# Kernel tuning notes

Measured on AMD Instinct MI355X. Metric: run time of the kernel, lower is better.

Reference implementation:

```python
import jax, jax.numpy as jnp
import numpy as np

N = 50000      # nodes
E = 800000     # edges (before self-loops)
F_IN = 128     # args.nsegment
H = 4          # args.nhead
C = 32         # args.dhidden
OUT = 64       # output_dim
G = 64         # number of graphs in batch
NEG = 0.2      # args.negslope (and GATv2 internal leaky-relu slope, PyG default 0.2)


def setup_inputs() -> dict:
    key = jax.random.key(0)
    ks = jax.random.split(key, 8)
    def w(k, i, o):
        return jax.random.normal(k, (i, o), jnp.float32) / np.sqrt(i)
    x = jax.random.normal(ks[0], (N, F_IN), jnp.float32)
    edge_index = jax.random.randint(ks[1], (2, E), 0, N, dtype=jnp.int32)
    batch = jnp.sort(jax.random.randint(ks[2], (N,), 0, G, dtype=jnp.int32))
    d = dict(x=x, edge_index=edge_index, batch=batch)
    # layer dims: (in_dim, heads, out_per_head, concat)
    dims = [(F_IN, H, C, True), (H * C, H, C, True), (H * C, 1, OUT, False)]
    for li, (fi, h, c, concat) in enumerate(dims):
        k1, k2, k3 = jax.random.split(ks[3 + li], 3)
        d[f"Wl{li}"] = w(k1, fi, h * c)
        d[f"Wr{li}"] = w(k2, fi, h * c)
        d[f"att{li}"] = jax.random.normal(k3, (h, c), jnp.float32) / np.sqrt(c)
        d[f"b{li}"] = jnp.zeros((h * c if concat else c,), jnp.float32)
    return d


def _gat_layer(x, src, tgt, Wl, Wr, att, b, concat):
    """GATv2Conv: e_ij = att . leaky_relu(Wl x_j + Wr x_i); softmax over edges into i;
    out_i = sum_j alpha_ij * (Wl x_j). src/tgt include self-loops."""
    n = x.shape[0]
    h, c = att.shape
    xl = (x @ Wl).reshape(n, h, c)                 # source transform [N,h,c]
    xr = (x @ Wr).reshape(n, h, c)                 # target transform [N,h,c]
    g = jax.nn.leaky_relu(xl[src] + xr[tgt], NEG)  # [Etot,h,c]
    score = jnp.einsum('ehc,hc->eh', g, att)       # [Etot,h]
    smax = jax.ops.segment_max(score, tgt, num_segments=n)
    ex = jnp.exp(score - smax[tgt])
    den = jax.ops.segment_sum(ex, tgt, num_segments=n)
    alpha = ex / den[tgt]                          # per-target softmax [Etot,h]
    out = jax.ops.segment_sum(xl[src] * alpha[:, :, None], tgt, num_segments=n)
    out = out.reshape(n, h * c) if concat else out.mean(axis=1)
    return out + b


def _forward(x, edge_index, batch, params):
    n = x.shape[0]
    loops = jnp.arange(n, dtype=edge_index.dtype)  # PyG add_self_loops=True
    src = jnp.concatenate([edge_index[0], loops])
    tgt = jnp.concatenate([edge_index[1], loops])
    for Wl, Wr, att, b, concat in params:
        x = _gat_layer(x, src, tgt, Wl, Wr, att, b, concat)
        x = jax.nn.leaky_relu(x, NEG)  # dropout p is identity in eval mode
    ssum = jax.ops.segment_sum(x, batch, num_segments=G)
    cnt = jax.ops.segment_sum(jnp.ones((n,), x.dtype), batch, num_segments=G)
    return ssum / jnp.maximum(cnt, 1.0)[:, None]   # global_mean_pool -> [G, OUT]


def reference(x, edge_index, batch, Wl0, Wr0, att0, b0, Wl1, Wr1, att1, b1, Wl2, Wr2, att2, b2):
    params = [(Wl0, Wr0, att0, b0, True),
              (Wl1, Wr1, att1, b1, True),
              (Wl2, Wr2, att2, b2, False)]
    return _forward(x, edge_index, batch, params)
```

## Files before the change

### kernel.cpp

```cpp
#include <hip/hip_runtime.h>
#include <hip/hip_fp16.h>
#include <math.h>

#define NEGSLOPE 0.2f

typedef _Float16 f16x8 __attribute__((ext_vector_type(8)));
typedef _Float16 f16x2 __attribute__((ext_vector_type(2)));
typedef float f32x4 __attribute__((ext_vector_type(4)));

__device__ __forceinline__ float lrelu(float x) { return x > 0.f ? x : NEGSLOPE * x; }

__device__ __forceinline__ float dot2acc(f16x2 a, f16x2 b, float c) {
#if __has_builtin(__builtin_amdgcn_fdot2)
    return __builtin_amdgcn_fdot2(a, b, c, false);
#else
    return c + (float)a[0] * (float)b[0] + (float)a[1] * (float)b[1];
#endif
}

__global__ __launch_bounds__(256) void k_prep(
        const float* __restrict__ x, _Float16* __restrict__ xh, int n8, int XB,
        const float* W0, const float* W1, const float* W2,
        const float* W3, const float* W4, const float* W5,
        _Float16* D0, _Float16* D1, _Float16* D2,
        _Float16* D3, _Float16* D4, _Float16* D5,
        int* __restrict__ zbase, int nzero) {
    int b = blockIdx.x, t = threadIdx.x;
    if (b < XB) {
        int i = b * 256 + t;
        if (i < n8) {
            float4 a = ((const float4*)x)[2 * i], c = ((const float4*)x)[2 * i + 1];
            union { uint4 u; _Float16 h[8]; } pk;
            pk.h[0] = (_Float16)a.x; pk.h[1] = (_Float16)a.y;
            pk.h[2] = (_Float16)a.z; pk.h[3] = (_Float16)a.w;
            pk.h[4] = (_Float16)c.x; pk.h[5] = (_Float16)c.y;
            pk.h[6] = (_Float16)c.z; pk.h[7] = (_Float16)c.w;
            ((uint4*)xh)[i] = pk.u;
        }
    } else if (b < XB + 320) {
        const float* Ws[6] = {W0, W1, W2, W3, W4, W5};
        _Float16* Ds[6] = {D0, D1, D2, D3, D4, D5};
        int j = (b - XB) * 256 + t;
        int m, jj, kout;
        if (j < 65536) { m = j >> 14; jj = j & 16383; kout = 128; }
        else           { m = 4 + ((j - 65536) >> 13); jj = (j - 65536) & 8191; kout = 64; }
        int col = jj >> 7, k = jj & 127;
        Ds[m][col * 128 + k] = (_Float16)Ws[m][k * kout + col];
    } else {
        int i = (b - XB - 320) * 256 + t;
        if (i < nzero) zbase[i] = 0;
    }
}

__global__ void k_count(const int* __restrict__ tgt, int* __restrict__ deg,
                        int* __restrict__ rank, int e) {
    int i = blockIdx.x * 256 + threadIdx.x;
    if (i < e) rank[i] = atomicAdd(&deg[tgt[i]], 1);
}
__global__ __launch_bounds__(256) void k_scanA(const int* __restrict__ deg, int* __restrict__ rowptr,
                                               int* __restrict__ bsums, int* __restrict__ bhist, int n) {
    __shared__ int s[256];
    __shared__ int lh[64];
    int t = threadIdx.x;
    if (t < 64) lh[t] = 0;
    int base = blockIdx.x * 4096 + t * 16;
    int pre[16];
    int sum = 0;
    __syncthreads();
    for (int i = 0; i < 16; ++i) {
        int idx = base + i;
        int v = 0;
        if (idx < n) {
            v = deg[idx] + 1;
            atomicAdd(&lh[v < 63 ? v : 63], 1);
        }
        pre[i] = sum;
        sum += v;
    }
    s[t] = sum;
    __syncthreads();
    for (int off = 1; off < 256; off <<= 1) {
        int v = (t >= off) ? s[t - off] : 0;
        __syncthreads();
        s[t] += v;
        __syncthreads();
    }
    int tbase = s[t] - sum;
    for (int i = 0; i < 16; ++i) {
        int idx = base + i;
        if (idx < n) rowptr[idx] = tbase + pre[i];
    }
    if (t == 0) bsums[blockIdx.x] = s[255];
    if (t < 64) bhist[blockIdx.x * 64 + t] = lh[t];
}
__global__ void k_binit(const int* __restrict__ bhist, int* __restrict__ boff, int nscan) {
    __shared__ int tots[64];
    __shared__ int base[64];
    int b = threadIdx.x;
    int tot = 0;
    for (int sb = 0; sb < nscan; ++sb) {
        boff[sb * 64 + b] = tot;
        tot += bhist[sb * 64 + b];
    }
    tots[b] = tot;
    __syncthreads();
    if (b == 0) {
        int run = 0;
        for (int k = 0; k < 64; ++k) { base[k] = run; run += tots[k]; }
    }
    __syncthreads();
    for (int sb = 0; sb < nscan; ++sb) boff[sb * 64 + b] += base[b];
}
__global__ __launch_bounds__(256) void k_scanC(int* __restrict__ rowptr, const int* __restrict__ bsums,
                                               int* __restrict__ edst, const int* __restrict__ deg,
                                               const int* __restrict__ boff, int* __restrict__ perm,
                                               int nscan, int n) {
    __shared__ int pref[17];
    __shared__ int cur[64];
    int t = threadIdx.x;
    if (t == 0) {
        int run = 0;
        for (int k = 0; k < nscan; ++k) { pref[k] = run; run += bsums[k]; }
        pref[nscan] = run;
    }
    if (t < 64) cur[t] = boff[blockIdx.x * 64 + t];
    __syncthreads();
    int myoff = pref[blockIdx.x];
    int base = blockIdx.x * 4096 + t * 16;
    for (int i = 0; i < 16; ++i) {
        int idx = base + i;
        if (idx < n) {
            int rp = rowptr[idx] + myoff;
            rowptr[idx] = rp;
            edst[rp] = idx;
            int d = deg[idx] + 1;
            int slot = atomicAdd(&cur[d < 63 ? d : 63], 1);
            perm[slot] = idx;
        }
    }
    if (blockIdx.x == gridDim.x - 1 && t == 0) rowptr[n] = pref[nscan];
}
__global__ void k_scatter(const int* __restrict__ src, const int* __restrict__ tgt,
                          const int* __restrict__ rank, const int* __restrict__ rowptr,
                          int* __restrict__ edst, int e) {
    int i = blockIdx.x * 256 + threadIdx.x;
    if (i < e) {
        int p = rowptr[tgt[i]] + 1 + rank[i];
        __builtin_nontemporal_store(src[i], &edst[p]);
    }
}

template<int KOUT>
__global__ __launch_bounds__(256) void k_gemm_mfma(
        const _Float16* __restrict__ Ah,
        const _Float16* __restrict__ Wt0, const _Float16* __restrict__ Wt1,
        _Float16* __restrict__ out0, _Float16* __restrict__ out1, int n) {
    int wv = threadIdx.x >> 6, lane = threadIdx.x & 63;
    int m = lane & 15, q = lane >> 4;
    int row0 = blockIdx.x * 128 + wv * 32;
    int ra = row0 + m, rb = row0 + 16 + m;
    if (ra >= n) ra = n - 1;
    if (rb >= n) rb = n - 1;
    const _Float16* apa = Ah + (size_t)ra * 128 + q * 8;
    const _Float16* apb = Ah + (size_t)rb * 128 + q * 8;

    const _Float16* Wp = Wt0;
    _Float16* outp = out0;
    if (KOUT == 128 && blockIdx.y) { Wp = Wt1; outp = out1; }

    f32x4 acc0[8] = {}, acc1[8] = {};
#pragma unroll
    for (int kt = 0; kt < 4; ++kt) {
        f16x8 wf[8];
#pragma unroll
        for (int ct = 0; ct < 8; ++ct) {
            const _Float16* W = (KOUT == 128) ? Wp : (ct < 4 ? Wt0 : Wt1);
            int col0 = (KOUT == 128) ? ct * 16 : (ct & 3) * 16;
            wf[ct] = *(const f16x8*)(W + (size_t)(col0 + m) * 128 + 32 * kt + 8 * q);
        }
        f16x8 bf0 = *(const f16x8*)(apa + 32 * kt);
        f16x8 bf1 = *(const f16x8*)(apb + 32 * kt);
#pragma unroll
        for (int ct = 0; ct < 8; ++ct) {
            acc0[ct] = __builtin_amdgcn_mfma_f32_16x16x32_f16(wf[ct], bf0, acc0[ct], 0, 0, 0);
            acc1[ct] = __builtin_amdgcn_mfma_f32_16x16x32_f16(wf[ct], bf1, acc1[ct], 0, 0, 0);
        }
    }
    int rowa = row0 + m, rowb = row0 + 16 + m;
#pragma unroll
    for (int ct = 0; ct < 8; ++ct) {
        _Float16* dst = (KOUT == 128) ? outp : (ct < 4 ? out0 : out1);
        int col = ((KOUT == 128) ? ct * 16 : (ct & 3) * 16) + q * 4;
        union { uint2 u; _Float16 h[4]; } pk;
        if (rowa < n) {
#pragma unroll
            for (int i = 0; i < 4; ++i) pk.h[i] = (_Float16)acc0[ct][i];
            *(uint2*)(dst + (size_t)rowa * KOUT + col) = pk.u;
        }
        if (rowb < n) {
#pragma unroll
            for (int i = 0; i < 4; ++i) pk.h[i] = (_Float16)acc1[ct][i];
            *(uint2*)(dst + (size_t)rowb * KOUT + col) = pk.u;
        }
    }
}

template<int H, int C, typename OutT>
__global__ __launch_bounds__(256) void k_agg(const _Float16* __restrict__ xl, const _Float16* __restrict__ xr,
                                             const float* __restrict__ att, const float* __restrict__ bias,
                                             const int* __restrict__ rowptr, const int* __restrict__ edst,
                                             const int* __restrict__ perm,
                                             OutT* __restrict__ yout, int n) {
    constexpr int F = H * C;
    constexpr int VEC = F / 16;
    constexpr int NH2 = VEC / 2;
    constexpr int L = C / VEC;
    int lane = threadIdx.x & 63;
    int wave = threadIdx.x >> 6;
    int s = lane & 15;
    int gid = blockIdx.x * 16 + wave * 4 + (lane >> 4);
    bool valid = gid < n;
    int node = valid ? perm[gid] : 0;
    int ch = s * VEC;

    f16x2 u2[NH2], av2[NH2];
    {
        union { uint4 u4; uint2 u2v; f16x2 h[4]; } pk;
        if constexpr (NH2 == 4) pk.u4 = *(const uint4*)(xr + (size_t)node * F + ch);
        else pk.u2v = *(const uint2*)(xr + (size_t)node * F + ch);
#pragma unroll
        for (int j = 0; j < NH2; ++j) u2[j] = pk.h[j];
    }
#pragma unroll
    for (int j = 0; j < NH2; ++j) {
        av2[j][0] = (_Float16)att[ch + 2 * j];
        av2[j][1] = (_Float16)att[ch + 2 * j + 1];
    }

    float acc[VEC];
#pragma unroll
    for (int j = 0; j < VEC; ++j) acc[j] = 0.f;
    int e0 = rowptr[node];
    int deg = valid ? (rowptr[node + 1] - e0) : 0;
    int maxdeg = deg;
    maxdeg = max(maxdeg, __shfl_xor(maxdeg, 16));
    maxdeg = max(maxdeg, __shfl_xor(maxdeg, 32));
    float ssum = 0.f;

    const _Float16 cneg = (_Float16)NEGSLOPE;
    auto edge = [&](int srcRow, bool live) {
        union { uint4 u4; uint2 u2v; f16x2 hh[4]; } pk;
        const _Float16* p = xl + (size_t)srcRow * F + ch;
        if constexpr (NH2 == 4) pk.u4 = *(const uint4*)p;
        else pk.u2v = *(const uint2*)p;
        float sc = 0.f;
#pragma unroll
        for (int j = 0; j < NH2; ++j) {
            f16x2 t = pk.hh[j] + u2[j];
            f16x2 lr = __builtin_elementwise_max(t, t * cneg);
            sc = dot2acc(lr, av2[j], sc);
        }
#pragma unroll
        for (int off = 1; off < L; off <<= 1) sc += __shfl_xor(sc, off);
        float w = live ? __expf(sc) : 0.f;
        ssum += w;
#pragma unroll
        for (int j = 0; j < NH2; ++j) {
            acc[2 * j]     += w * (float)pk.hh[j][0];
            acc[2 * j + 1] += w * (float)pk.hh[j][1];
        }
    };

    for (int base = 0; base < maxdeg; base += 16) {
        int cnt = deg - base;
        if (cnt > 16) cnt = 16;
        int idxreg = (s < cnt) ? edst[e0 + base + s] : node;
        int mcnt = cnt;
        mcnt = max(mcnt, __shfl_xor(mcnt, 16));
        mcnt = max(mcnt, __shfl_xor(mcnt, 32));
        int gbase = lane & 48;
        int i = 0;
        for (; i + 2 <= mcnt; i += 2) {
            int s0 = __shfl(idxreg, gbase + i);
            int s1 = __shfl(idxreg, gbase + i + 1);
            edge(s0, i < cnt);
            edge(s1, i + 1 < cnt);
        }
        for (; i < mcnt; ++i) {
            int s0 = __shfl(idxreg, gbase + i);
            edge(s0, i < cnt);
        }
    }
    if (valid) {
        float inv = 1.f / ssum;
        float o[VEC];
#pragma unroll
        for (int j = 0; j < VEC; ++j) o[j] = lrelu(acc[j] * inv + bias[ch + j]);
        if constexpr (sizeof(OutT) == 2) {
            _Float16* p = (_Float16*)yout + (size_t)node * F + ch;
            if constexpr (VEC == 8) {
                union { uint4 u; _Float16 h[8]; } pk;
#pragma unroll
                for (int j = 0; j < 8; ++j) pk.h[j] = (_Float16)o[j];
                *(uint4*)p = pk.u;
            } else {
                union { uint2 u; _Float16 h[4]; } pk;
#pragma unroll
                for (int j = 0; j < 4; ++j) pk.h[j] = (_Float16)o[j];
                *(uint2*)p = pk.u;
            }
        } else {
            float* p = (float*)yout + (size_t)node * F + ch;
            *(float4*)p = make_float4(o[0], o[1], o[2], o[3]);
            if constexpr (VEC == 8)
                *(float4*)(p + 4) = make_float4(o[4], o[5], o[6], o[7]);
        }
    }
}

__global__ __launch_bounds__(256) void k_pool_partial(const float* __restrict__ y,
        const int* __restrict__ batch, float* __restrict__ pacc, int n, int nchunk) {
    __shared__ float sdata[256];
    __shared__ int range[2];
    int g = blockIdx.x;
    int chunk = blockIdx.y;
    int t = threadIdx.x;
    if (t == 0) {
        int lo = 0, hi = n;
        while (lo < hi) { int mid = (lo + hi) >> 1; if (batch[mid] < g) lo = mid + 1; else hi = mid; }
        range[0] = lo;
        hi = n;
        while (lo < hi) { int mid = (lo + hi) >> 1; if (batch[mid] < g + 1) lo = mid + 1; else hi = mid; }
        range[1] = lo;
    }
    __syncthreads();
    int start = range[0], len = range[1] - range[0];
    int lo = start + (int)((long long)len * chunk / nchunk);
    int hi = start + (int)((long long)len * (chunk + 1) / nchunk);
    int ch = t & 63, sub = t >> 6;
    float acc = 0.f;
    for (int node = lo + sub; node < hi; node += 4)
        acc += y[(size_t)node * 64 + ch];
    sdata[t] = acc;
    __syncthreads();
    if (t < 128) sdata[t] += sdata[t + 128];
    __syncthreads();
    if (t < 64) atomicAdd(&pacc[g * 64 + t], sdata[t] + sdata[t + 64]);
}
__global__ void k_pool_final(const float* __restrict__ pacc, const int* __restrict__ batch,
                             float* __restrict__ out, int n) {
    __shared__ int cntS;
    int g = blockIdx.x, t = threadIdx.x;
    if (t == 0) {
        int lo = 0, hi = n;
        while (lo < hi) { int mid = (lo + hi) >> 1; if (batch[mid] < g) lo = mid + 1; else hi = mid; }
        int s = lo;
        hi = n;
        while (lo < hi) { int mid = (lo + hi) >> 1; if (batch[mid] < g + 1) lo = mid + 1; else hi = mid; }
        cntS = lo - s;
    }
    __syncthreads();
    out[g * 64 + t] = pacc[g * 64 + t] / fmaxf((float)cntS, 1.f);
}

extern "C" void kernel_launch(void* const* d_in, const int* in_sizes, int n_in,
                              void* d_out, int out_size, void* d_ws, size_t ws_size,
                              hipStream_t stream) {
    const float* x     = (const float*)d_in[0];
    const int*   ei    = (const int*)d_in[1];
    const int*   batch = (const int*)d_in[2];
    const float* Wl0 = (const float*)d_in[3];
    const float* Wr0 = (const float*)d_in[4];
    const float* att0 = (const float*)d_in[5];
    const float* b0  = (const float*)d_in[6];
    const float* Wl1 = (const float*)d_in[7];
    const float* Wr1 = (const float*)d_in[8];
    const float* att1 = (const float*)d_in[9];
    const float* b1  = (const float*)d_in[10];
    const float* Wl2 = (const float*)d_in[11];
    const float* Wr2 = (const float*)d_in[12];
    const float* att2 = (const float*)d_in[13];
    const float* b2  = (const float*)d_in[14];

    const int N = in_sizes[2];
    const int E = in_sizes[1] / 2;
    const int G = out_size / 64;
    const int* src = ei;
    const int* tgt = ei + E;

    size_t off = 0;
    auto take = [&](size_t bytes) {
        void* p = (char*)d_ws + off;
        off = (off + bytes + 255) & ~(size_t)255;
        return p;
    };
    _Float16* xh   = (_Float16*)take((size_t)N * 128 * 2);
    _Float16* Ah   = (_Float16*)take((size_t)N * 128 * 2);
    _Float16* B    = (_Float16*)take((size_t)N * 128 * 2);
    _Float16* Cbh  = (_Float16*)take((size_t)N * 128 * 2);
    float* Cbf     = (float*)take((size_t)N * 64 * 4);
    _Float16* Wl0t = (_Float16*)take(128 * 128 * 2);
    _Float16* Wr0t = (_Float16*)take(128 * 128 * 2);
    _Float16* Wl1t = (_Float16*)take(128 * 128 * 2);
    _Float16* Wr1t = (_Float16*)take(128 * 128 * 2);
    _Float16* Wl2t = (_Float16*)take(64 * 128 * 2);
    _Float16* Wr2t = (_Float16*)take(64 * 128 * 2);
    int* rowptr = (int*)take((size_t)(N + 1) * 4);
    int* tmp    = (int*)take((size_t)N * 4);
    float* pacc = (float*)take((size_t)G * 64 * 4);
    int* bhist  = (int*)take(16 * 64 * 4);
    int* boff   = (int*)take(16 * 64 * 4);
    int* perm   = (int*)take((size_t)N * 4);
    int* rank   = (int*)take((size_t)E * 4);
    int* edst   = (int*)take((size_t)(E + N) * 4);
    int* bsums  = (int*)take(64 * 4);
    (void)ws_size; (void)n_in;

    const int TB = 256;
    int nblkE = (E + TB - 1) / TB;
    int nscan = (N + 4095) / 4096;

    int n8 = N * 128 / 8;
    int XB = (n8 + TB - 1) / TB;
    int nzero = (int)(((char*)bhist) - (char*)tmp) / 4;
    int ZB = (nzero + TB - 1) / TB;
    k_prep<<<XB + 320 + ZB, TB, 0, stream>>>(x, xh, n8, XB,
        Wl0, Wr0, Wl1, Wr1, Wl2, Wr2,
        Wl0t, Wr0t, Wl1t, Wr1t, Wl2t, Wr2t,
        tmp, nzero);

    k_count<<<nblkE, TB, 0, stream>>>(tgt, tmp, rank, E);
    k_scanA<<<nscan, TB, 0, stream>>>(tmp, rowptr, bsums, bhist, N);
    k_binit<<<1, 64, 0, stream>>>(bhist, boff, nscan);
    k_scanC<<<nscan, TB, 0, stream>>>(rowptr, bsums, edst, tmp, boff, perm, nscan, N);
    k_scatter<<<nblkE, TB, 0, stream>>>(src, tgt, rank, rowptr, edst, E);

    int gemmBlocks = (N + 127) / 128;
    dim3 gemmGrid2(gemmBlocks, 2);
    dim3 gemmGrid1(gemmBlocks, 1);
    int aggBlocks = (N + 15) / 16;

    k_gemm_mfma<128><<<gemmGrid2, TB, 0, stream>>>(xh, Wl0t, Wr0t, Ah, B, N);
    k_agg<4, 32, _Float16><<<aggBlocks, TB, 0, stream>>>(Ah, B, att0, b0, rowptr, edst, perm, Cbh, N);

    k_gemm_mfma<128><<<gemmGrid2, TB, 0, stream>>>(Cbh, Wl1t, Wr1t, Ah, B, N);
    k_agg<4, 32, _Float16><<<aggBlocks, TB, 0, stream>>>(Ah, B, att1, b1, rowptr, edst, perm, Cbh, N);

    k_gemm_mfma<64><<<gemmGrid1, TB, 0, stream>>>(Cbh, Wl2t, Wr2t, Ah, B, N);
    k_agg<1, 64, float><<<aggBlocks, TB, 0, stream>>>(Ah, B, att2, b2, rowptr, edst, perm, Cbf, N);

    dim3 poolGrid(G, 16);
    k_pool_partial<<<poolGrid, TB, 0, stream>>>(Cbf, batch, pacc, N, 16);
    k_pool_final<<<G, 64, 0, stream>>>(pacc, batch, (float*)d_out, N);
}
```

Baseline: 358.4 us.

## Fuse fp32 input cast into first GEMM, merge bucket init, unroll edge loads

The first-layer GEMM now reads the fp32 node features directly and converts them to fp16 in registers. This removes the separate cast pass and the fp16 copy of x in the workspace. The single-block k_binit kernel is folded into k_scanC, with each block recomputing the bucket offsets from bhist, which saves one launch. The aggregation inner loop now issues four gathered row loads before processing them, to expose more memory-level parallelism. In exchange, the GEMM reads twice as many bytes for layer 0 (x is read once per grid.y slice), and the aggregation kernel uses more registers.

```diff
diff --git a/kernel.cpp b/kernel.cpp
--- a/kernel.cpp
+++ b/kernel.cpp
@@ -19,35 +19,23 @@
 }
 
 __global__ __launch_bounds__(256) void k_prep(
-        const float* __restrict__ x, _Float16* __restrict__ xh, int n8, int XB,
         const float* W0, const float* W1, const float* W2,
         const float* W3, const float* W4, const float* W5,
         _Float16* D0, _Float16* D1, _Float16* D2,
         _Float16* D3, _Float16* D4, _Float16* D5,
         int* __restrict__ zbase, int nzero) {
     int b = blockIdx.x, t = threadIdx.x;
-    if (b < XB) {
-        int i = b * 256 + t;
-        if (i < n8) {
-            float4 a = ((const float4*)x)[2 * i], c = ((const float4*)x)[2 * i + 1];
-            union { uint4 u; _Float16 h[8]; } pk;
-            pk.h[0] = (_Float16)a.x; pk.h[1] = (_Float16)a.y;
-            pk.h[2] = (_Float16)a.z; pk.h[3] = (_Float16)a.w;
-            pk.h[4] = (_Float16)c.x; pk.h[5] = (_Float16)c.y;
-            pk.h[6] = (_Float16)c.z; pk.h[7] = (_Float16)c.w;
-            ((uint4*)xh)[i] = pk.u;
-        }
-    } else if (b < XB + 320) {
+    if (b < 320) {
         const float* Ws[6] = {W0, W1, W2, W3, W4, W5};
         _Float16* Ds[6] = {D0, D1, D2, D3, D4, D5};
-        int j = (b - XB) * 256 + t;
+        int j = b * 256 + t;
         int m, jj, kout;
         if (j < 65536) { m = j >> 14; jj = j & 16383; kout = 128; }
         else           { m = 4 + ((j - 65536) >> 13); jj = (j - 65536) & 8191; kout = 64; }
         int col = jj >> 7, k = jj & 127;
         Ds[m][col * 128 + k] = (_Float16)Ws[m][k * kout + col];
     } else {
-        int i = (b - XB - 320) * 256 + t;
+        int i = (b - 320) * 256 + t;
         if (i < nzero) zbase[i] = 0;
     }
 }
@@ -93,37 +81,36 @@
     if (t == 0) bsums[blockIdx.x] = s[255];
     if (t < 64) bhist[blockIdx.x * 64 + t] = lh[t];
 }
-__global__ void k_binit(const int* __restrict__ bhist, int* __restrict__ boff, int nscan) {
-    __shared__ int tots[64];
-    __shared__ int base[64];
-    int b = threadIdx.x;
-    int tot = 0;
-    for (int sb = 0; sb < nscan; ++sb) {
-        boff[sb * 64 + b] = tot;
-        tot += bhist[sb * 64 + b];
-    }
-    tots[b] = tot;
-    __syncthreads();
-    if (b == 0) {
-        int run = 0;
-        for (int k = 0; k < 64; ++k) { base[k] = run; run += tots[k]; }
-    }
-    __syncthreads();
-    for (int sb = 0; sb < nscan; ++sb) boff[sb * 64 + b] += base[b];
-}
 __global__ __launch_bounds__(256) void k_scanC(int* __restrict__ rowptr, const int* __restrict__ bsums,
                                                int* __restrict__ edst, const int* __restrict__ deg,
-                                               const int* __restrict__ boff, int* __restrict__ perm,
+                                               const int* __restrict__ bhist, int* __restrict__ perm,
                                                int nscan, int n) {
     __shared__ int pref[17];
     __shared__ int cur[64];
+    __shared__ int bbase[64];
     int t = threadIdx.x;
     if (t == 0) {
         int run = 0;
         for (int k = 0; k < nscan; ++k) { pref[k] = run; run += bsums[k]; }
         pref[nscan] = run;
     }
-    if (t < 64) cur[t] = boff[blockIdx.x * 64 + t];
+    if (t < 64) {
+        int part = 0, tot = 0;
+        for (int sb = 0; sb < nscan; ++sb) {
+            int v = bhist[sb * 64 + t];
+            if (sb < (int)blockIdx.x) part += v;
+            tot += v;
+        }
+        bbase[t] = tot;
+        cur[t] = part;
+    }
+    __syncthreads();
+    if (t == 0) {
+        int run = 0;
+        for (int k = 0; k < 64; ++k) { int v = bbase[k]; bbase[k] = run; run += v; }
+    }
+    __syncthreads();
+    if (t < 64) cur[t] += bbase[t];
     __syncthreads();
     int myoff = pref[blockIdx.x];
     int base = blockIdx.x * 4096 + t * 16;
@@ -150,9 +137,9 @@
     }
 }
 
-template<int KOUT>
+template<int KOUT, typename AT>
 __global__ __launch_bounds__(256) void k_gemm_mfma(
-        const _Float16* __restrict__ Ah,
+        const AT* __restrict__ Ah,
         const _Float16* __restrict__ Wt0, const _Float16* __restrict__ Wt1,
         _Float16* __restrict__ out0, _Float16* __restrict__ out1, int n) {
     int wv = threadIdx.x >> 6, lane = threadIdx.x & 63;
@@ -161,8 +148,20 @@
     int ra = row0 + m, rb = row0 + 16 + m;
     if (ra >= n) ra = n - 1;
     if (rb >= n) rb = n - 1;
-    const _Float16* apa = Ah + (size_t)ra * 128 + q * 8;
-    const _Float16* apb = Ah + (size_t)rb * 128 + q * 8;
+    const AT* apa = Ah + (size_t)ra * 128 + q * 8;
+    const AT* apb = Ah + (size_t)rb * 128 + q * 8;
+
+    auto loadB = [](const AT* p) -> f16x8 {
+        if constexpr (sizeof(AT) == 2) {
+            return *(const f16x8*)p;
+        } else {
+            float4 a = *(const float4*)p, b = *(const float4*)(p + 4);
+            f16x8 r;
+            r[0] = (_Float16)a.x; r[1] = (_Float16)a.y; r[2] = (_Float16)a.z; r[3] = (_Float16)a.w;
+            r[4] = (_Float16)b.x; r[5] = (_Float16)b.y; r[6] = (_Float16)b.z; r[7] = (_Float16)b.w;
+            return r;
+        }
+    };
 
     const _Float16* Wp = Wt0;
     _Float16* outp = out0;
@@ -178,8 +177,8 @@
             int col0 = (KOUT == 128) ? ct * 16 : (ct & 3) * 16;
             wf[ct] = *(const f16x8*)(W + (size_t)(col0 + m) * 128 + 32 * kt + 8 * q);
         }
-        f16x8 bf0 = *(const f16x8*)(apa + 32 * kt);
-        f16x8 bf1 = *(const f16x8*)(apb + 32 * kt);
+        f16x8 bf0 = loadB(apa + 32 * kt);
+        f16x8 bf1 = loadB(apb + 32 * kt);
 #pragma unroll
         for (int ct = 0; ct < 8; ++ct) {
             acc0[ct] = __builtin_amdgcn_mfma_f32_16x16x32_f16(wf[ct], bf0, acc0[ct], 0, 0, 0);
@@ -223,13 +222,15 @@
     int node = valid ? perm[gid] : 0;
     int ch = s * VEC;
 
+    union PkU { uint4 u4; uint2 u2v; f16x2 hh[4]; };
+
     f16x2 u2[NH2], av2[NH2];
     {
-        union { uint4 u4; uint2 u2v; f16x2 h[4]; } pk;
+        PkU pk;
         if constexpr (NH2 == 4) pk.u4 = *(const uint4*)(xr + (size_t)node * F + ch);
         else pk.u2v = *(const uint2*)(xr + (size_t)node * F + ch);
 #pragma unroll
-        for (int j = 0; j < NH2; ++j) u2[j] = pk.h[j];
+        for (int j = 0; j < NH2; ++j) u2[j] = pk.hh[j];
     }
 #pragma unroll
     for (int j = 0; j < NH2; ++j) {
@@ -248,11 +249,12 @@
     float ssum = 0.f;
 
     const _Float16 cneg = (_Float16)NEGSLOPE;
-    auto edge = [&](int srcRow, bool live) {
-        union { uint4 u4; uint2 u2v; f16x2 hh[4]; } pk;
+    auto loadrow = [&](int srcRow, PkU& pk) {
         const _Float16* p = xl + (size_t)srcRow * F + ch;
         if constexpr (NH2 == 4) pk.u4 = *(const uint4*)p;
         else pk.u2v = *(const uint2*)p;
+    };
+    auto process = [&](PkU& pk, bool live) {
         float sc = 0.f;
 #pragma unroll
         for (int j = 0; j < NH2; ++j) {
@@ -280,15 +282,23 @@
         mcnt = max(mcnt, __shfl_xor(mcnt, 32));
         int gbase = lane & 48;
         int i = 0;
-        for (; i + 2 <= mcnt; i += 2) {
+        for (; i + 4 <= mcnt; i += 4) {
             int s0 = __shfl(idxreg, gbase + i);
             int s1 = __shfl(idxreg, gbase + i + 1);
-            edge(s0, i < cnt);
-            edge(s1, i + 1 < cnt);
+            int s2 = __shfl(idxreg, gbase + i + 2);
+            int s3 = __shfl(idxreg, gbase + i + 3);
+            PkU p0, p1, p2, p3;
+            loadrow(s0, p0); loadrow(s1, p1); loadrow(s2, p2); loadrow(s3, p3);
+            process(p0, i < cnt);
+            process(p1, i + 1 < cnt);
+            process(p2, i + 2 < cnt);
+            process(p3, i + 3 < cnt);
         }
         for (; i < mcnt; ++i) {
             int s0 = __shfl(idxreg, gbase + i);
-            edge(s0, i < cnt);
+            PkU p0;
+            loadrow(s0, p0);
+            process(p0, i < cnt);
         }
     }
     if (valid) {
@@ -394,7 +404,6 @@
         off = (off + bytes + 255) & ~(size_t)255;
         return p;
     };
-    _Float16* xh   = (_Float16*)take((size_t)N * 128 * 2);
     _Float16* Ah   = (_Float16*)take((size_t)N * 128 * 2);
     _Float16* B    = (_Float16*)take((size_t)N * 128 * 2);
     _Float16* Cbh  = (_Float16*)take((size_t)N * 128 * 2);
@@ -409,7 +418,6 @@
     int* tmp    = (int*)take((size_t)N * 4);
     float* pacc = (float*)take((size_t)G * 64 * 4);
     int* bhist  = (int*)take(16 * 64 * 4);
-    int* boff   = (int*)take(16 * 64 * 4);
     int* perm   = (int*)take((size_t)N * 4);
     int* rank   = (int*)take((size_t)E * 4);
     int* edst   = (int*)take((size_t)(E + N) * 4);
@@ -420,19 +428,16 @@
     int nblkE = (E + TB - 1) / TB;
     int nscan = (N + 4095) / 4096;
 
-    int n8 = N * 128 / 8;
-    int XB = (n8 + TB - 1) / TB;
     int nzero = (int)(((char*)bhist) - (char*)tmp) / 4;
     int ZB = (nzero + TB - 1) / TB;
-    k_prep<<<XB + 320 + ZB, TB, 0, stream>>>(x, xh, n8, XB,
+    k_prep<<<320 + ZB, TB, 0, stream>>>(
         Wl0, Wr0, Wl1, Wr1, Wl2, Wr2,
         Wl0t, Wr0t, Wl1t, Wr1t, Wl2t, Wr2t,
         tmp, nzero);
 
     k_count<<<nblkE, TB, 0, stream>>>(tgt, tmp, rank, E);
     k_scanA<<<nscan, TB, 0, stream>>>(tmp, rowptr, bsums, bhist, N);
-    k_binit<<<1, 64, 0, stream>>>(bhist, boff, nscan);
-    k_scanC<<<nscan, TB, 0, stream>>>(rowptr, bsums, edst, tmp, boff, perm, nscan, N);
+    k_scanC<<<nscan, TB, 0, stream>>>(rowptr, bsums, edst, tmp, bhist, perm, nscan, N);
     k_scatter<<<nblkE, TB, 0, stream>>>(src, tgt, rank, rowptr, edst, E);
 
     int gemmBlocks = (N + 127) / 128;
@@ -440,13 +445,13 @@
     dim3 gemmGrid1(gemmBlocks, 1);
     int aggBlocks = (N + 15) / 16;
 
-    k_gemm_mfma<128><<<gemmGrid2, TB, 0, stream>>>(xh, Wl0t, Wr0t, Ah, B, N);
+    k_gemm_mfma<128, float><<<gemmGrid2, TB, 0, stream>>>(x, Wl0t, Wr0t, Ah, B, N);
     k_agg<4, 32, _Float16><<<aggBlocks, TB, 0, stream>>>(Ah, B, att0, b0, rowptr, edst, perm, Cbh, N);
 
-    k_gemm_mfma<128><<<gemmGrid2, TB, 0, stream>>>(Cbh, Wl1t, Wr1t, Ah, B, N);
+    k_gemm_mfma<128, _Float16><<<gemmGrid2, TB, 0, stream>>>(Cbh, Wl1t, Wr1t, Ah, B, N);
     k_agg<4, 32, _Float16><<<aggBlocks, TB, 0, stream>>>(Ah, B, att1, b1, rowptr, edst, perm, Cbh, N);
 
-    k_gemm_mfma<64><<<gemmGrid1, TB, 0, stream>>>(Cbh, Wl2t, Wr2t, Ah, B, N);
+    k_gemm_mfma<64, _Float16><<<gemmGrid1, TB, 0, stream>>>(Cbh, Wl2t, Wr2t, Ah, B, N);
     k_agg<1, 64, float><<<aggBlocks, TB, 0, stream>>>(Ah, B, att2, b2, rowptr, edst, perm, Cbf, N);
 
     dim3 poolGrid(G, 16);
```

Result: no change. 358.3 us (median of 2 runs) (-0.0%).
